# Kernel tuning notes

Hardware: AMD Instinct MI355X
Metric: run time of the kernel (lower is better)

Reference implementation:

```python
import jax, jax.numpy as jnp
import numpy as np

B, N, C, H = 2, 2048, 1024, 16
D = C // H          # head_dim = 64
HALF = D // 2       # 32 complex pairs per head


def setup_inputs() -> dict:
    key = jax.random.key(0)
    k1, k2, k3, k4 = jax.random.split(key, 4)
    x = jax.random.normal(k1, (B, N, C), dtype=jnp.float32)
    # 0.02 init scale keeps softmax logits in a sane range
    qkv_w = jax.random.normal(k2, (3 * C, C), dtype=jnp.float32) * 0.02
    proj_w = jax.random.normal(k3, (C, C), dtype=jnp.float32) * 0.02
    proj_b = jax.random.normal(k4, (C,), dtype=jnp.float32) * 0.02
    # standard RoPE frequencies: theta = 10000^{-2i/D}
    inv_freq = 1.0 / (10000.0 ** (jnp.arange(0, D, 2, dtype=jnp.float32) / D))
    angles = jnp.arange(N, dtype=jnp.float32)[:, None] * inv_freq[None, :]  # [N, HALF]
    return {
        "x": x, "qkv_w": qkv_w, "proj_w": proj_w, "proj_b": proj_b,
        "freqs_cos": jnp.cos(angles), "freqs_sin": jnp.sin(angles),
    }


def _rope(t, cos, sin):
    # t: [B, N, H, D]; cos/sin: [N, HALF] -> broadcast as [1, N, 1, HALF]
    tr = t.reshape(B, N, H, HALF, 2)
    t_re, t_im = tr[..., 0], tr[..., 1]
    c = cos[None, :, None, :]
    s = sin[None, :, None, :]
    o_re = t_re * c - t_im * s
    o_im = t_re * s + t_im * c
    return jnp.stack([o_re, o_im], axis=-1).reshape(B, N, H, D)


def reference(x, qkv_w, proj_w, proj_b, freqs_cos, freqs_sin):
    scale = D ** -0.5
    qkv = x @ qkv_w.T                              # [B, N, 3C] (no bias: qkv_bias=False)
    qkv = qkv.reshape(B, N, 3, H, D)
    q, k, v = qkv[:, :, 0], qkv[:, :, 1], qkv[:, :, 2]  # [B, N, H, D]
    q = _rope(q, freqs_cos, freqs_sin)
    k = _rope(k, freqs_cos, freqs_sin)
    scores = jnp.einsum("bqhd,bkhd->bhqk", q, k) * scale
    attn = jax.nn.softmax(scores, axis=-1)         # dropout p=0.0 -> identity
    out = jnp.einsum("bhqk,bkhd->bqhd", attn, v).reshape(B, N, C)
    return out @ proj_w.T + proj_b
```

## Files before the change

kernel.cpp:

```cpp
#include <hip/hip_runtime.h>
#include <hip/hip_bf16.h>

#define B_ 2
#define N_ 2048
#define C_ 1024
#define H_ 16
#define D_ 64
#define HALF_ 32

typedef __attribute__((ext_vector_type(8))) __bf16 bf16x8;
typedef __attribute__((ext_vector_type(8))) unsigned short u16x8;
typedef __attribute__((ext_vector_type(4))) float f32x4;
typedef __attribute__((ext_vector_type(16))) float f32x16;

__device__ __forceinline__ unsigned short f2bf(float f) {
  union { float f; unsigned u; } v; v.f = f;
  unsigned r = v.u + 0x7FFFu + ((v.u >> 16) & 1u);
  return (unsigned short)(r >> 16);
}

__device__ __forceinline__ unsigned cvt_pk_bf16(float lo, float hi) {
  unsigned r;
  asm("v_cvt_pk_bf16_f32 %0, %1, %2" : "=v"(r) : "v"(lo), "v"(hi));
  return r;
}

__device__ __forceinline__ void gload_lds16(const void* g, void* l) {
  __builtin_amdgcn_global_load_lds(
      (const __attribute__((address_space(1))) void*)g,
      (__attribute__((address_space(3))) void*)l, 16, 0, 0);
}

__global__ __launch_bounds__(256) void cast3_f32_bf16(
    const float* __restrict__ a, const float* __restrict__ b,
    const float* __restrict__ c, unsigned short* __restrict__ oa,
    unsigned short* __restrict__ ob, unsigned short* __restrict__ oc) {
  int i = blockIdx.x * 256 + threadIdx.x;
  const float4* src;
  ushort4* dst;
  int off;
  if (i < 1048576) {
    src = (const float4*)a; dst = (ushort4*)oa; off = i;
  } else if (i < 1835008) {
    src = (const float4*)b; dst = (ushort4*)ob; off = i - 1048576;
  } else {
    src = (const float4*)c; dst = (ushort4*)oc; off = i - 1835008;
  }
  float4 v = src[off];
  ushort4 o;
  o.x = f2bf(v.x); o.y = f2bf(v.y); o.z = f2bf(v.z); o.w = f2bf(v.w);
  dst[off] = o;
}

template <int EPI>
__global__ __launch_bounds__(256) void gemm_bt(
    const unsigned short* __restrict__ A, const unsigned short* __restrict__ Bw,
    int M, int Nn, int K,
    float* __restrict__ Cout, const float* __restrict__ bias,
    unsigned short* __restrict__ qo, unsigned short* __restrict__ ko,
    unsigned short* __restrict__ vto,
    const float* __restrict__ cosT, const float* __restrict__ sinT) {
  __shared__ __align__(16) unsigned short As[128][64];
  __shared__ __align__(16) unsigned short Bs[128][64];
  const int tid = threadIdx.x;
  const int lane = tid & 63;
  const int wid = tid >> 6;
  const int wm = wid >> 1, wn = wid & 1;
  const int l15 = lane & 15;
  const int g = lane >> 4;

  const int per = gridDim.x >> 3;
  const int f = blockIdx.x;
  const int nat = (f & 7) * per + (f >> 3);
  const int mtiles = M >> 7;
  const int m0 = (nat % mtiles) * 128;
  const int n0 = (nat / mtiles) * 128;

  const int srow = wid * 8 + (lane >> 3);
  const int scol = (lane & 7) * 8;

  f32x4 acc[4][4] = {};

  const int nK = K >> 6;
  for (int kt = 0; kt < nK; ++kt) {
    __syncthreads();
#pragma unroll
    for (int j = 0; j < 4; ++j) {
      gload_lds16(&A[(size_t)(m0 + j * 32 + srow) * K + kt * 64 + scol],
                  &As[j * 32 + wid * 8][0]);
      gload_lds16(&Bw[(size_t)(n0 + j * 32 + srow) * K + kt * 64 + scol],
                  &Bs[j * 32 + wid * 8][0]);
    }
    __syncthreads();
#pragma unroll
    for (int kk = 0; kk < 2; ++kk) {
      bf16x8 af[4], bfv[4];
#pragma unroll
      for (int m = 0; m < 4; ++m)
        af[m] = *reinterpret_cast<const bf16x8*>(&As[wm * 64 + m * 16 + l15][kk * 32 + g * 8]);
#pragma unroll
      for (int n = 0; n < 4; ++n)
        bfv[n] = *reinterpret_cast<const bf16x8*>(&Bs[wn * 64 + n * 16 + l15][kk * 32 + g * 8]);
#pragma unroll
      for (int m = 0; m < 4; ++m)
#pragma unroll
        for (int n = 0; n < 4; ++n)
          acc[m][n] = __builtin_amdgcn_mfma_f32_16x16x32_bf16(af[m], bfv[n], acc[m][n], 0, 0, 0);
    }
  }

  if constexpr (EPI == 0) {
#pragma unroll
    for (int n = 0; n < 4; ++n) {
      int col = n0 + wn * 64 + n * 16 + l15;
      float bv = bias[col];
#pragma unroll
      for (int m = 0; m < 4; ++m) {
        int rbase = m0 + wm * 64 + m * 16 + g * 4;
#pragma unroll
        for (int r = 0; r < 4; ++r)
          Cout[(size_t)(rbase + r) * Nn + col] = acc[m][n][r] + bv;
      }
    }
  } else {
    const int which = n0 >> 10;
    if (which == 2) {
#pragma unroll
      for (int m = 0; m < 4; ++m)
#pragma unroll
        for (int n = 0; n < 4; ++n) {
          int col = n0 + wn * 64 + n * 16 + l15;
          int hc = col & 1023;
          int hh = hc >> 6, d = hc & 63;
          int row0 = m0 + wm * 64 + m * 16 + g * 4;
          int seq0 = row0 & (N_ - 1), bb = row0 >> 11;
          int seqP = (seq0 & ~12) | ((seq0 & 4) << 1) | ((seq0 & 8) >> 1);
          ushort4 pk;
          pk.x = f2bf(acc[m][n][0]); pk.y = f2bf(acc[m][n][1]);
          pk.z = f2bf(acc[m][n][2]); pk.w = f2bf(acc[m][n][3]);
          *reinterpret_cast<ushort4*>(
              &vto[(((size_t)bb * H_ + hh) * D_ + d) * N_ + seqP]) = pk;
        }
    } else {
      unsigned short* dst = (which == 0) ? qo : ko;
      const float qscale = (which == 0) ? 0.125f * 1.44269504f : 1.0f;
#pragma unroll
      for (int m = 0; m < 4; ++m)
#pragma unroll
        for (int n = 0; n < 4; ++n)
#pragma unroll
          for (int r = 0; r < 4; ++r) {
            int col = n0 + wn * 64 + n * 16 + l15;
            int row = m0 + wm * 64 + m * 16 + g * 4 + r;
            float val = acc[m][n][r];
            float partner = __shfl_xor(val, 1);
            int hc = col & 1023;
            int hh = hc >> 6, d = hc & 63;
            int seq = row & (N_ - 1), bb = row >> 11;
            float cs = cosT[seq * HALF_ + (d >> 1)];
            float sn = sinT[seq * HALF_ + (d >> 1)];
            float res = (d & 1) ? (partner * sn + val * cs) : (val * cs - partner * sn);
            res *= qscale;
            dst[(((size_t)bb * H_ + hh) * N_ + seq) * D_ + d] = f2bf(res);
          }
    }
  }
}

__global__ __launch_bounds__(512) void attn_kernel(
    const unsigned short* __restrict__ q,
    const unsigned short* __restrict__ k,
    const unsigned short* __restrict__ vt,
    unsigned short* __restrict__ o) {
  __shared__ __align__(16) unsigned short Kl[2][64][64];
  __shared__ __align__(16) unsigned short Vl[2][64][64];

  const int tid = threadIdx.x;
  const int lane = tid & 63;
  const int w = tid >> 6;
  const int l31 = lane & 31;
  const int hi = lane >> 5;

  const int bid = blockIdx.x;
  const int nat = (bid & 7) * 32 + (bid >> 3);
  const int qt = nat & 7;
  const int bh = nat >> 3;
  const int b = bh >> 4, h = bh & 15;

  const size_t hk = (size_t)bh * N_ * D_;
  const size_t hv = (size_t)bh * D_ * N_;
  const int qrow = qt * 256 + w * 32 + l31;

  bf16x8 qf[4];
#pragma unroll
  for (int kt = 0; kt < 4; ++kt)
    qf[kt] = *reinterpret_cast<const bf16x8*>(
        &q[hk + (size_t)qrow * D_ + kt * 16 + hi * 8]);

  const int prow = tid >> 3;
  const int pchk = tid & 7;
  const int swz = (pchk ^ (prow & 7)) * 8;

  u16x8 kr, vr;
  auto issueK = [&](int t) {
    kr = *reinterpret_cast<const u16x8*>(&k[hk + (size_t)(t * 64 + prow) * D_ + pchk * 8]);
  };
  auto issueV = [&](int t) {
    vr = *reinterpret_cast<const u16x8*>(&vt[hv + (size_t)prow * N_ + t * 64 + pchk * 8]);
  };
  auto commitK = [&](int buf) { *reinterpret_cast<u16x8*>(&Kl[buf][prow][swz]) = kr; };
  auto commitV = [&](int buf) { *reinterpret_cast<u16x8*>(&Vl[buf][prow][swz]) = vr; };

  f32x16 accO[2] = {};
  float lrun = 0.f;
  const int b7 = l31 & 7;
  const int NT = N_ / 64;

  f32x16 sA[2], sB[2];

#define QK_MFMA(T, SC)                                                        \
  do {                                                                        \
    f32x16 z_ = {};                                                           \
    SC[0] = z_; SC[1] = z_;                                                   \
    __builtin_amdgcn_s_setprio(1);                                            \
    _Pragma("unroll")                                                         \
    for (int kb = 0; kb < 2; ++kb)                                            \
      _Pragma("unroll")                                                       \
      for (int kt = 0; kt < 4; ++kt) {                                        \
        bf16x8 kf = *reinterpret_cast<const bf16x8*>(                         \
            &Kl[(T) & 1][kb * 32 + l31][(((kt * 2 + hi) ^ b7)) * 8]);         \
        SC[kb] = __builtin_amdgcn_mfma_f32_32x32x16_bf16(kf, qf[kt], SC[kb], 0, 0, 0); \
      }                                                                       \
    __builtin_amdgcn_s_setprio(0);                                            \
  } while (0)

#define SMPV(SP, VB)                                                          \
  do {                                                                        \
    _Pragma("unroll")                                                         \
    for (int kb = 0; kb < 2; ++kb)                                            \
      _Pragma("unroll")                                                       \
      for (int i = 0; i < 16; ++i) SP[kb][i] = __builtin_exp2f(SP[kb][i]);    \
    float sloc[16];                                                           \
    _Pragma("unroll")                                                         \
    for (int i = 0; i < 16; ++i) sloc[i] = SP[0][i] + SP[1][i];               \
    _Pragma("unroll")                                                         \
    for (int st = 8; st > 0; st >>= 1)                                        \
      _Pragma("unroll")                                                       \
      for (int i = 0; i < 8; ++i)                                             \
        if (i < st) sloc[i] += sloc[i + st];                                  \
    {                                                                         \
      unsigned ua = __float_as_uint(sloc[0]), ub = ua;                        \
      auto rr = __builtin_amdgcn_permlane32_swap(ua, ub, false, false);       \
      lrun += __uint_as_float(rr[0]) + __uint_as_float(rr[1]);                \
    }                                                                         \
    bf16x8 PA[4];                                                             \
    _Pragma("unroll")                                                         \
    for (int kvc = 0; kvc < 4; ++kvc) {                                       \
      const int kb = kvc >> 1, base = (kvc & 1) * 8;                          \
      union { unsigned u[4]; bf16x8 v; } pa;                                  \
      _Pragma("unroll")                                                       \
      for (int wd = 0; wd < 4; ++wd)                                          \
        pa.u[wd] = cvt_pk_bf16(SP[kb][base + 2 * wd], SP[kb][base + 2 * wd + 1]); \
      PA[kvc] = pa.v;                                                         \
    }                                                                         \
    __builtin_amdgcn_s_setprio(1);                                            \
    _Pragma("unroll")                                                         \
    for (int db = 0; db < 2; ++db)                                            \
      _Pragma("unroll")                                                       \
      for (int kvc = 0; kvc < 4; ++kvc) {                                     \
        bf16x8 vf = *reinterpret_cast<const bf16x8*>(                         \
            &Vl[VB][db * 32 + l31][(((kvc * 2 + hi) ^ b7)) * 8]);             \
        accO[db] = __builtin_amdgcn_mfma_f32_32x32x16_bf16(vf, PA[kvc], accO[db], 0, 0, 0); \
      }                                                                       \
    __builtin_amdgcn_s_setprio(0);                                            \
  } while (0)

#define BODY(T, SP, SC)                                                       \
  do {                                                                        \
    const int t_ = (T);                                                       \
    if (t_ + 1 < NT) issueK(t_ + 1);                                          \
    issueV(t_);                                                               \
    QK_MFMA(t_, SC);                                                          \
    SMPV(SP, (t_ - 1) & 1);                                                   \
    if (t_ + 1 < NT) commitK((t_ + 1) & 1);                                   \
    commitV(t_ & 1);                                                          \
    __syncthreads();                                                          \
  } while (0)

  issueK(0);
  commitK(0);
  __syncthreads();

  issueK(1);
  issueV(0);
  QK_MFMA(0, sA);
  commitK(1);
  commitV(0);
  __syncthreads();

  for (int tt = 1; tt + 1 < NT; tt += 2) {
    BODY(tt, sA, sB);
    BODY(tt + 1, sB, sA);
  }
  BODY(NT - 1, sA, sB);

  SMPV(sB, (NT - 1) & 1);

  float rl = 1.0f / lrun;
  const size_t obase = ((size_t)b * N_ + qrow) * C_ + h * 64;
#pragma unroll
  for (int db = 0; db < 2; ++db)
#pragma unroll
    for (int rg = 0; rg < 4; ++rg) {
      ushort4 pk;
      pk.x = f2bf(accO[db][rg * 4 + 0] * rl);
      pk.y = f2bf(accO[db][rg * 4 + 1] * rl);
      pk.z = f2bf(accO[db][rg * 4 + 2] * rl);
      pk.w = f2bf(accO[db][rg * 4 + 3] * rl);
      *reinterpret_cast<ushort4*>(&o[obase + db * 32 + rg * 8 + hi * 4]) = pk;
    }
#undef BODY
#undef SMPV
#undef QK_MFMA
}

extern "C" void kernel_launch(void* const* d_in, const int* in_sizes, int n_in,
                              void* d_out, int out_size, void* d_ws, size_t ws_size,
                              hipStream_t stream) {
  const float* x      = (const float*)d_in[0];
  const float* qkv_w  = (const float*)d_in[1];
  const float* proj_w = (const float*)d_in[2];
  const float* proj_b = (const float*)d_in[3];
  const float* cosT   = (const float*)d_in[4];
  const float* sinT   = (const float*)d_in[5];
  float* out = (float*)d_out;

  unsigned short* xb     = (unsigned short*)d_ws;
  unsigned short* wqkvb  = xb + (size_t)4096 * 1024;
  unsigned short* wprojb = wqkvb + (size_t)3072 * 1024;
  unsigned short* qb     = wprojb + (size_t)1024 * 1024;
  unsigned short* kb     = qb + (size_t)32 * 2048 * 64;
  unsigned short* vtb    = kb + (size_t)32 * 2048 * 64;
  unsigned short* ab     = vtb + (size_t)32 * 2048 * 64;

  cast3_f32_bf16<<<8192, 256, 0, stream>>>(x, qkv_w, proj_w, xb, wqkvb, wprojb);

  gemm_bt<1><<<768, 256, 0, stream>>>(xb, wqkvb, 4096, 3072, 1024,
                                      nullptr, nullptr, qb, kb, vtb, cosT, sinT);

  attn_kernel<<<256, 512, 0, stream>>>(qb, kb, vtb, ab);

  gemm_bt<0><<<256, 256, 0, stream>>>(ab, wprojb, 4096, 1024, 1024,
                                      out, proj_b, nullptr, nullptr, nullptr,
                                      nullptr, nullptr);
}
```

Baseline: 147.9 us.

## Double-buffer GEMM LDS tiles with async prefetch and interleave cos/sin table

```diff
diff --git a/kernel.cpp b/kernel.cpp
--- a/kernel.cpp
+++ b/kernel.cpp
@@ -34,8 +34,15 @@
 __global__ __launch_bounds__(256) void cast3_f32_bf16(
     const float* __restrict__ a, const float* __restrict__ b,
     const float* __restrict__ c, unsigned short* __restrict__ oa,
-    unsigned short* __restrict__ ob, unsigned short* __restrict__ oc) {
+    unsigned short* __restrict__ ob, unsigned short* __restrict__ oc,
+    const float* __restrict__ cosT, const float* __restrict__ sinT,
+    float2* __restrict__ csT) {
   int i = blockIdx.x * 256 + threadIdx.x;
+  if (i >= 2097152) {
+    int i2 = i - 2097152;
+    csT[i2] = make_float2(cosT[i2], sinT[i2]);
+    return;
+  }
   const float4* src;
   ushort4* dst;
   int off;
@@ -59,9 +66,9 @@
     float* __restrict__ Cout, const float* __restrict__ bias,
     unsigned short* __restrict__ qo, unsigned short* __restrict__ ko,
     unsigned short* __restrict__ vto,
-    const float* __restrict__ cosT, const float* __restrict__ sinT) {
-  __shared__ __align__(16) unsigned short As[128][64];
-  __shared__ __align__(16) unsigned short Bs[128][64];
+    const float2* __restrict__ csT) {
+  __shared__ __align__(16) unsigned short As[2][128][64];
+  __shared__ __align__(16) unsigned short Bs[2][128][64];
   const int tid = threadIdx.x;
   const int lane = tid & 63;
   const int wid = tid >> 6;
@@ -79,34 +86,45 @@
   const int srow = wid * 8 + (lane >> 3);
   const int scol = (lane & 7) * 8;
 
-  f32x4 acc[4][4] = {};
-
-  const int nK = K >> 6;
-  for (int kt = 0; kt < nK; ++kt) {
-    __syncthreads();
+  auto stage = [&](int kt, int buf) {
 #pragma unroll
     for (int j = 0; j < 4; ++j) {
       gload_lds16(&A[(size_t)(m0 + j * 32 + srow) * K + kt * 64 + scol],
-                  &As[j * 32 + wid * 8][0]);
+                  &As[buf][j * 32 + wid * 8][0]);
       gload_lds16(&Bw[(size_t)(n0 + j * 32 + srow) * K + kt * 64 + scol],
-                  &Bs[j * 32 + wid * 8][0]);
-    }
-    __syncthreads();
+                  &Bs[buf][j * 32 + wid * 8][0]);
+    }
+  };
+
+  f32x4 acc[4][4] = {};
+
+  const int nK = K >> 6;
+  stage(0, 0);
+  stage(1, 1);
+
+  for (int kt = 0; kt < nK; ++kt) {
+    const int buf = kt & 1;
+    if (kt == nK - 1) asm volatile("s_waitcnt vmcnt(0)" ::: "memory");
+    else              asm volatile("s_waitcnt vmcnt(8)" ::: "memory");
+    __builtin_amdgcn_s_barrier();
+    __builtin_amdgcn_sched_barrier(0);
 #pragma unroll
     for (int kk = 0; kk < 2; ++kk) {
       bf16x8 af[4], bfv[4];
 #pragma unroll
       for (int m = 0; m < 4; ++m)
-        af[m] = *reinterpret_cast<const bf16x8*>(&As[wm * 64 + m * 16 + l15][kk * 32 + g * 8]);
+        af[m] = *reinterpret_cast<const bf16x8*>(&As[buf][wm * 64 + m * 16 + l15][kk * 32 + g * 8]);
 #pragma unroll
       for (int n = 0; n < 4; ++n)
-        bfv[n] = *reinterpret_cast<const bf16x8*>(&Bs[wn * 64 + n * 16 + l15][kk * 32 + g * 8]);
+        bfv[n] = *reinterpret_cast<const bf16x8*>(&Bs[buf][wn * 64 + n * 16 + l15][kk * 32 + g * 8]);
 #pragma unroll
       for (int m = 0; m < 4; ++m)
 #pragma unroll
         for (int n = 0; n < 4; ++n)
           acc[m][n] = __builtin_amdgcn_mfma_f32_16x16x32_bf16(af[m], bfv[n], acc[m][n], 0, 0, 0);
     }
+    __builtin_amdgcn_s_barrier();
+    if (kt + 2 < nK) stage(kt + 2, buf);
   }
 
   if constexpr (EPI == 0) {
@@ -157,9 +175,8 @@
             int hc = col & 1023;
             int hh = hc >> 6, d = hc & 63;
             int seq = row & (N_ - 1), bb = row >> 11;
-            float cs = cosT[seq * HALF_ + (d >> 1)];
-            float sn = sinT[seq * HALF_ + (d >> 1)];
-            float res = (d & 1) ? (partner * sn + val * cs) : (val * cs - partner * sn);
+            float2 cs = csT[seq * HALF_ + (d >> 1)];
+            float res = (d & 1) ? (partner * cs.y + val * cs.x) : (val * cs.x - partner * cs.y);
             res *= qscale;
             dst[(((size_t)bb * H_ + hh) * N_ + seq) * D_ + d] = f2bf(res);
           }
@@ -342,15 +359,17 @@
   unsigned short* kb     = qb + (size_t)32 * 2048 * 64;
   unsigned short* vtb    = kb + (size_t)32 * 2048 * 64;
   unsigned short* ab     = vtb + (size_t)32 * 2048 * 64;
-
-  cast3_f32_bf16<<<8192, 256, 0, stream>>>(x, qkv_w, proj_w, xb, wqkvb, wprojb);
+  float2* csT            = (float2*)(ab + (size_t)4096 * 1024);
+
+  cast3_f32_bf16<<<8448, 256, 0, stream>>>(x, qkv_w, proj_w, xb, wqkvb, wprojb,
+                                           cosT, sinT, csT);
 
   gemm_bt<1><<<768, 256, 0, stream>>>(xb, wqkvb, 4096, 3072, 1024,
-                                      nullptr, nullptr, qb, kb, vtb, cosT, sinT);
+                                      nullptr, nullptr, qb, kb, vtb, csT);
 
   attn_kernel<<<256, 512, 0, stream>>>(qb, kb, vtb, ab);
 
   gemm_bt<0><<<256, 256, 0, stream>>>(ab, wprojb, 4096, 1024, 1024,
                                       out, proj_b, nullptr, nullptr, nullptr,
-                                      nullptr, nullptr);
-}
+                                      csT);
+}
```

Measured after the change: 141.3 us. 4.5% less time.
